# Kernel optimization log

Hardware: AMD Instinct MI355X
Metric: run time of the kernel (lower is better)

## Reference

```python
import jax, jax.numpy as jnp
import numpy as np

N_NODES = 400000
N_EDGES = 800000
N_GRAPHS = 16384
IN_DIM = 78
GNN_DIMS = [128, 128, 128]
FF_DIMS = [256, 128]


def _glorot(key, shape):
    fan_in, fan_out = shape
    lim = np.sqrt(6.0 / (fan_in + fan_out))
    return jax.random.uniform(key, shape, jnp.float32, -lim, lim)


def setup_inputs() -> dict:
    key = jax.random.key(0)
    ks = jax.random.split(key, 16)
    x = jax.random.normal(ks[0], (N_NODES, IN_DIM), jnp.float32)
    edge_index = jax.random.randint(ks[1], (2, N_EDGES), 0, N_NODES, jnp.int64)
    batch = jnp.sort(jax.random.randint(ks[2], (N_NODES,), 0, N_GRAPHS, jnp.int64))
    d = dict(x=x, edge_index=edge_index, batch=batch, n_graphs=N_GRAPHS)
    dims = [IN_DIM] + GNN_DIMS
    for i in range(3):
        d[f'gW{i}'] = _glorot(ks[3 + i], (dims[i], dims[i + 1]))
        d[f'gb{i}'] = jnp.zeros((dims[i + 1],), jnp.float32)
    fdims = [GNN_DIMS[-1]] + FF_DIMS
    for i in range(2):
        d[f'fW{i}'] = _glorot(ks[8 + i], (fdims[i], fdims[i + 1]))
        d[f'fb{i}'] = jnp.zeros((fdims[i + 1],), jnp.float32)
    return d


def gcn_conv(x, src, dst, deg_isqrt, W, b, n_nodes):
    # GCNConv: linear first, then propagate with sym norm over A + I
    h = x @ W  # [N, D]
    norm = (deg_isqrt[src] * deg_isqrt[dst])[:, None]  # [E, 1]
    msg = h[src] * norm  # [E, D] gather
    out = jax.ops.segment_sum(msg, dst, num_segments=n_nodes)  # scatter-add
    # self-loop contribution: norm_ii = deg_i^-1
    out = out + h * (deg_isqrt * deg_isqrt)[:, None]
    return out + b


def reference(x, edge_index, batch, n_graphs,
              gW0, gb0, gW1, gb1, gW2, gb2,
              fW0, fb0, fW1, fb1):
    n_nodes = x.shape[0]
    src, dst = edge_index[0], edge_index[1]
    # degree of A + I on target side
    deg = 1.0 + jax.ops.segment_sum(jnp.ones((src.shape[0],), x.dtype), dst,
                                    num_segments=n_nodes)
    deg_isqrt = jax.lax.rsqrt(deg)
    for W, b in ((gW0, gb0), (gW1, gb1), (gW2, gb2)):
        x = jax.nn.relu(gcn_conv(x, src, dst, deg_isqrt, W, b, n_nodes))
    # global max pool per graph (empty segments -> 0; x >= 0 post-ReLU)
    pooled = jax.ops.segment_max(x, batch, num_segments=n_graphs)
    pooled = jnp.where(jnp.isfinite(pooled), pooled, 0.0)
    # FF head: Linear -> ReLU -> Dropout(eval: identity)
    h = jax.nn.relu(pooled @ fW0 + fb0)
    h = jax.nn.relu(h @ fW1 + fb1)
    return h
```

## Files before the change

kernel.cpp:

```cpp
#include <hip/hip_runtime.h>

#define NN 400000
#define NE 800000
#define NG 16384

typedef short bf16x8 __attribute__((ext_vector_type(8)));
typedef float f32x4 __attribute__((ext_vector_type(4)));
typedef unsigned short u16x8 __attribute__((ext_vector_type(8)));

static inline int cdiv(int a, int b) { return (a + b - 1) / b; }

__device__ inline unsigned short bf16_rne(float v) {
    unsigned u = __float_as_uint(v);
    unsigned r = u + 0x7FFFu + ((u >> 16) & 1u);
    return (unsigned short)(r >> 16);
}
__device__ inline float bf16_to_f(unsigned short h) {
    return __uint_as_float(((unsigned)h) << 16);
}
__device__ inline void split2(float v, unsigned short& hi, unsigned short& lo) {
    hi = bf16_rne(v);
    lo = bf16_rne(v - bf16_to_f(hi));
}

__global__ __launch_bounds__(256) void fill_kernel(float* __restrict__ p, float v, int n) {
    int i = blockIdx.x * blockDim.x + threadIdx.x;
    if (i < n) p[i] = v;
}

__global__ __launch_bounds__(256) void fill_int_kernel(int* __restrict__ p, int v, int n) {
    int i = blockIdx.x * blockDim.x + threadIdx.x;
    if (i < n) p[i] = v;
}

__global__ __launch_bounds__(256) void hist_kernel(const int* __restrict__ dst,
                                                   int* __restrict__ deg, int E) {
    int e = blockIdx.x * blockDim.x + threadIdx.x;
    if (e < E) atomicAdd(&deg[dst[e]], 1);
}

__global__ __launch_bounds__(256) void disq_kernel(const int* __restrict__ deg,
                                                   float* __restrict__ disq, int n) {
    int i = blockIdx.x * blockDim.x + threadIdx.x;
    if (i < n) disq[i] = rsqrtf(1.0f + (float)deg[i]);
}

#define SCAN_TPB 256
#define SCAN_EPT 8
#define SCAN_BE (SCAN_TPB * SCAN_EPT)

__global__ __launch_bounds__(SCAN_TPB) void scan_a_kernel(const int* __restrict__ in,
                                                          int* __restrict__ out,
                                                          int* __restrict__ partials, int n) {
    __shared__ int sums[SCAN_TPB];
    const int tid = threadIdx.x;
    int base = blockIdx.x * SCAN_BE + tid * SCAN_EPT;
    int v[SCAN_EPT];
    int s = 0;
#pragma unroll
    for (int i = 0; i < SCAN_EPT; ++i) {
        int idx = base + i;
        int x = (idx < n) ? in[idx] : 0;
        v[i] = s;
        s += x;
    }
    sums[tid] = s;
    __syncthreads();
    for (int off = 1; off < SCAN_TPB; off <<= 1) {
        int t = (tid >= off) ? sums[tid - off] : 0;
        __syncthreads();
        sums[tid] += t;
        __syncthreads();
    }
    int toff = (tid == 0) ? 0 : sums[tid - 1];
#pragma unroll
    for (int i = 0; i < SCAN_EPT; ++i) {
        int idx = base + i;
        if (idx < n) out[idx] = toff + v[i];
    }
    if (tid == SCAN_TPB - 1) partials[blockIdx.x] = sums[SCAN_TPB - 1];
}

__global__ void scan_b_kernel(int* __restrict__ partials, int nb) {
    if (blockIdx.x == 0 && threadIdx.x == 0) {
        int s = 0;
        for (int i = 0; i < nb; ++i) { int x = partials[i]; partials[i] = s; s += x; }
    }
}

__global__ __launch_bounds__(256) void scan_c_kernel(int* __restrict__ out,
                                                     const int* __restrict__ partials, int n) {
    int idx = blockIdx.x * blockDim.x + threadIdx.x;
    if (idx < n) out[idx] += partials[idx / SCAN_BE];
}

__global__ __launch_bounds__(256) void csr_fill_kernel(const int* __restrict__ src,
                                                       const int* __restrict__ dst,
                                                       const int* __restrict__ rowptr,
                                                       int* __restrict__ cnt,
                                                       const float* __restrict__ disq,
                                                       int2* __restrict__ csr_ent, int E) {
    int e = blockIdx.x * blockDim.x + threadIdx.x;
    if (e >= E) return;
    int d = dst[e], s = src[e];
    int pos = rowptr[d] + atomicAdd(&cnt[d], 1);
    csr_ent[pos] = make_int2(s, __float_as_int(disq[s] * disq[d]));
}

__global__ __launch_bounds__(256) void prep_w_kernel(const float* __restrict__ W, int K,
                                                     unsigned short* __restrict__ planeHi,
                                                     unsigned short* __restrict__ planeLo) {
    int i = blockIdx.x * blockDim.x + threadIdx.x;
    if (i >= 128 * 128) return;
    int n = i >> 7, k = i & 127;
    float v = (k < K) ? W[k * 128 + n] : 0.0f;
    unsigned short hi, lo;
    split2(v, hi, lo);
    int elem = (n * 256 + ((2 * k) ^ ((n & 7) << 4))) >> 1;
    planeHi[elem] = hi;
    planeLo[elem] = lo;
}

__global__ __launch_bounds__(256) void xconv_kernel(const float* __restrict__ x,
                                                    unsigned short* __restrict__ xbf) {
    long long t = (long long)blockIdx.x * blockDim.x + threadIdx.x;
    if (t >= (long long)NN * 96) return;
    int node = (int)(t / 96), k = (int)(t - (long long)node * 96);
    float v = (k < 78) ? x[(size_t)node * 78 + k] : 0.0f;
    xbf[(size_t)node * 96 + k] = bf16_rne(v);
}

template <int STRIDE>
__global__ __launch_bounds__(256) void gather_kernel(const unsigned short* __restrict__ act,
                                                     const int* __restrict__ rowptr,
                                                     const int* __restrict__ deg,
                                                     const int2* __restrict__ csr_ent,
                                                     const float* __restrict__ disq,
                                                     unsigned short* __restrict__ aggHi, int n) {
    int t = blockIdx.x * blockDim.x + threadIdx.x;
    if (t >= n * 16) return;
    int node = t >> 4, q = (t & 15) * 8;
    const bool live = q < STRIDE;
    const int qc = live ? q : 0;
    int beg = rowptr[node];
    int d = deg[node];
    float si = disq[node];
    float s2 = si * si;
    u16x8 su = *reinterpret_cast<const u16x8*>(act + (size_t)node * STRIDE + qc);
    float acc[8];
#pragma unroll
    for (int i = 0; i < 8; ++i) acc[i] = bf16_to_f(su[i]) * s2;
    if (d > 0) {
        int lim = d - 1;
        int2 e[6];
#pragma unroll
        for (int j = 0; j < 6; ++j) e[j] = csr_ent[beg + (j < lim ? j : lim)];
        u16x8 u[6];
        float nr[6];
#pragma unroll
        for (int j = 0; j < 6; ++j) {
            u[j] = *reinterpret_cast<const u16x8*>(act + (size_t)e[j].x * STRIDE + qc);
            nr[j] = (j < d) ? __int_as_float(e[j].y) : 0.0f;
        }
#pragma unroll
        for (int j = 0; j < 6; ++j)
#pragma unroll
            for (int i = 0; i < 8; ++i) acc[i] = fmaf(bf16_to_f(u[j][i]), nr[j], acc[i]);
        for (int j = 6; j < d; ++j) {
            int2 ee = csr_ent[beg + j];
            float nn = __int_as_float(ee.y);
            u16x8 uu = *reinterpret_cast<const u16x8*>(act + (size_t)ee.x * STRIDE + qc);
#pragma unroll
            for (int i = 0; i < 8; ++i) acc[i] = fmaf(bf16_to_f(uu[i]), nn, acc[i]);
        }
    }
    if (live) {
        u16x8 h8;
#pragma unroll
        for (int i = 0; i < 8; ++i) h8[i] = bf16_rne(acc[i]);
        *reinterpret_cast<u16x8*>(aggHi + (size_t)node * STRIDE + q) = h8;
    }
}

template <int NKC, int AS>
__global__ __launch_bounds__(256) void gemm_mfma_kernel(const unsigned short* __restrict__ A,
                                                        const unsigned short* __restrict__ WT,
                                                        const float* __restrict__ bias,
                                                        unsigned short* __restrict__ act, int M) {
    __shared__ unsigned short lds[2 * 128 * 128];
    const int tid = threadIdx.x;
    {
        const unsigned* s = reinterpret_cast<const unsigned*>(WT);
        unsigned* d = reinterpret_cast<unsigned*>(lds);
#pragma unroll
        for (int i = 0; i < 64; ++i) d[tid + 256 * i] = s[tid + 256 * i];
    }
    __syncthreads();

    const int w = tid >> 6, lane = tid & 63;
    const int m = lane & 15, kb = lane >> 4;
    const char* ldsHiB = reinterpret_cast<const char*>(lds);
    const char* ldsLoB = ldsHiB + 128 * 256;

    float bcol[8];
#pragma unroll
    for (int ct = 0; ct < 8; ++ct) bcol[ct] = bias[ct * 16 + m];

    const int RT = 4;
    for (int rt = 0; rt < RT; ++rt) {
        int row0 = (blockIdx.x * RT + rt) * 64;
        if (row0 >= M) return;
        int arow = row0 + w * 16 + m;

        bf16x8 ah[NKC];
#pragma unroll
        for (int kc = 0; kc < NKC; ++kc)
            ah[kc] = *reinterpret_cast<const bf16x8*>(A + (size_t)arow * AS + kc * 32 + kb * 8);

        f32x4 acc[8];
#pragma unroll
        for (int ct = 0; ct < 8; ++ct)
#pragma unroll
            for (int r = 0; r < 4; ++r) acc[ct][r] = 0.0f;

#pragma unroll
        for (int ct = 0; ct < 8; ++ct) {
            int n = ct * 16 + m;
            int swz = (n & 7) << 4;
            int rowb = n * 256;
#pragma unroll
            for (int kc = 0; kc < NKC; ++kc) {
                int bb = rowb + ((kc * 64 + kb * 16) ^ swz);
                bf16x8 bh = *reinterpret_cast<const bf16x8*>(ldsHiB + bb);
                bf16x8 bl = *reinterpret_cast<const bf16x8*>(ldsLoB + bb);
                acc[ct] = __builtin_amdgcn_mfma_f32_16x16x32_bf16(ah[kc], bh, acc[ct], 0, 0, 0);
                acc[ct] = __builtin_amdgcn_mfma_f32_16x16x32_bf16(ah[kc], bl, acc[ct], 0, 0, 0);
            }
        }

        unsigned short* ap = act + (size_t)(row0 + w * 16) * 128;
#pragma unroll
        for (int ct = 0; ct < 8; ++ct)
#pragma unroll
            for (int r = 0; r < 4; ++r) {
                float v = fmaxf(acc[ct][r] + bcol[ct], 0.0f);
                ap[(size_t)(kb * 4 + r) * 128 + ct * 16 + m] = bf16_rne(v);
            }
    }
}

template <bool RELU_A, bool EPI>
__global__ __launch_bounds__(256) void gemm_kernel(const float* __restrict__ A,
                                                   const float* __restrict__ B,
                                                   const float* __restrict__ bias,
                                                   float* __restrict__ C,
                                                   int M, int N, int K) {
    const int BM = 64, BN = 64, BK = 16;
    __shared__ float As[BK][BM + 4];
    __shared__ float Bs[BK][BN + 4];

    const int tid = threadIdx.x;
    const int bm = blockIdx.x * BM;
    const int bn = blockIdx.y * BN;
    const int tx = tid & 15;
    const int ty = tid >> 4;

    const int arow = tid >> 2;
    const int acol = (tid & 3) * 4;
    const int brow = tid >> 4;
    const int bcol = (tid & 15) * 4;

    float acc[4][4] = {};

    for (int k0 = 0; k0 < K; k0 += BK) {
        {
            const float* ap = A + (size_t)(bm + arow) * K;
#pragma unroll
            for (int j = 0; j < 4; ++j) {
                int kk = k0 + acol + j;
                float v = (kk < K) ? ap[kk] : 0.0f;
                if (RELU_A) v = fmaxf(v, 0.0f);
                As[acol + j][arow] = v;
            }
        }
        {
            int kk = k0 + brow;
            float4 v = make_float4(0.f, 0.f, 0.f, 0.f);
            if (kk < K) v = *reinterpret_cast<const float4*>(B + (size_t)kk * N + bn + bcol);
            *reinterpret_cast<float4*>(&Bs[brow][bcol]) = v;
        }
        __syncthreads();
#pragma unroll
        for (int k = 0; k < BK; ++k) {
            float4 a4 = *reinterpret_cast<const float4*>(&As[k][ty * 4]);
            float4 b4 = *reinterpret_cast<const float4*>(&Bs[k][tx * 4]);
            float av[4] = {a4.x, a4.y, a4.z, a4.w};
            float bv[4] = {b4.x, b4.y, b4.z, b4.w};
#pragma unroll
            for (int i = 0; i < 4; ++i)
#pragma unroll
                for (int j = 0; j < 4; ++j)
                    acc[i][j] = fmaf(av[i], bv[j], acc[i][j]);
        }
        __syncthreads();
    }

    const int crow0 = bm + ty * 4;
    const int ccol0 = bn + tx * 4;
    float4 bv = make_float4(0.f, 0.f, 0.f, 0.f);
    if (EPI) bv = *reinterpret_cast<const float4*>(bias + ccol0);
#pragma unroll
    for (int i = 0; i < 4; ++i) {
        float4 v = make_float4(acc[i][0], acc[i][1], acc[i][2], acc[i][3]);
        if (EPI) {
            v.x = fmaxf(v.x + bv.x, 0.f);
            v.y = fmaxf(v.y + bv.y, 0.f);
            v.z = fmaxf(v.z + bv.z, 0.f);
            v.w = fmaxf(v.w + bv.w, 0.f);
        }
        *reinterpret_cast<float4*>(C + (size_t)(crow0 + i) * N + ccol0) = v;
    }
}

__global__ __launch_bounds__(256) void pool_kernel(const unsigned short* __restrict__ act,
                                                   const int* __restrict__ batch,
                                                   int* __restrict__ pooled, int n) {
    int t = blockIdx.x * blockDim.x + threadIdx.x;
    int d = t & 127;
    int n0 = (t >> 7) * 8;
    if (n0 >= n) return;
    int cur = batch[n0];
    float m = fmaxf(bf16_to_f(act[(size_t)n0 * 128 + d]), 0.f);
    for (int i = 1; i < 8 && (n0 + i) < n; ++i) {
        int b = batch[n0 + i];
        float v = fmaxf(bf16_to_f(act[(size_t)(n0 + i) * 128 + d]), 0.f);
        if (b == cur) {
            m = fmaxf(m, v);
        } else {
            atomicMax(&pooled[cur * 128 + d], __float_as_int(m));
            cur = b;
            m = v;
        }
    }
    atomicMax(&pooled[cur * 128 + d], __float_as_int(m));
}

extern "C" void kernel_launch(void* const* d_in, const int* in_sizes, int n_in,
                              void* d_out, int out_size, void* d_ws, size_t ws_size,
                              hipStream_t stream) {
    const float* x    = (const float*)d_in[0];
    const int*   edge = (const int*)d_in[1];
    const int*   batch= (const int*)d_in[2];
    const float* gW0  = (const float*)d_in[4];
    const float* gb0  = (const float*)d_in[5];
    const float* gW1  = (const float*)d_in[6];
    const float* gb1  = (const float*)d_in[7];
    const float* gW2  = (const float*)d_in[8];
    const float* gb2  = (const float*)d_in[9];
    const float* fW0  = (const float*)d_in[10];
    const float* fb0  = (const float*)d_in[11];
    const float* fW1  = (const float*)d_in[12];
    const float* fb1  = (const float*)d_in[13];
    float* out = (float*)d_out;

    unsigned short* actB  = (unsigned short*)d_ws;
    unsigned short* aggHi = actB + (size_t)NN * 128;
    float* disq   = (float*)(aggHi + (size_t)NN * 128);
    float* pooled = disq + NN;
    float* ffh    = pooled + (size_t)NG * 128;
    int*   deg    = (int*)(ffh + (size_t)NG * 256);
    int*   rowptr = deg + NN;
    int2*  csr_ent = (int2*)(rowptr + NN);
    unsigned short* wt0 = (unsigned short*)(csr_ent + NE);
    unsigned short* wt1 = wt0 + 2 * 128 * 128;
    unsigned short* wt2 = wt1 + 2 * 128 * 128;
    int* partials = (int*)(wt2 + 2 * 128 * 128);
    int* cnt = (int*)pooled;
    unsigned short* xbf = actB;

    const int* src = edge;
    const int* dst = edge + NE;

    fill_int_kernel<<<cdiv(NN, 256), 256, 0, stream>>>(deg, 0, NN);
    fill_int_kernel<<<cdiv(NN, 256), 256, 0, stream>>>(cnt, 0, NN);
    hist_kernel<<<cdiv(NE, 256), 256, 0, stream>>>(dst, deg, NE);
    disq_kernel<<<cdiv(NN, 256), 256, 0, stream>>>(deg, disq, NN);
    int nsb = cdiv(NN, SCAN_BE);
    scan_a_kernel<<<nsb, SCAN_TPB, 0, stream>>>(deg, rowptr, partials, NN);
    scan_b_kernel<<<1, 64, 0, stream>>>(partials, nsb);
    scan_c_kernel<<<cdiv(NN, 256), 256, 0, stream>>>(rowptr, partials, NN);
    csr_fill_kernel<<<cdiv(NE, 256), 256, 0, stream>>>(src, dst, rowptr, cnt, disq,
                                                       csr_ent, NE);
    prep_w_kernel<<<64, 256, 0, stream>>>(gW0, 78, wt0, wt0 + 128 * 128);
    prep_w_kernel<<<64, 256, 0, stream>>>(gW1, 128, wt1, wt1 + 128 * 128);
    prep_w_kernel<<<64, 256, 0, stream>>>(gW2, 128, wt2, wt2 + 128 * 128);
    xconv_kernel<<<cdiv(NN * 96, 256), 256, 0, stream>>>(x, xbf);

    const int gemm_blocks = cdiv(NN / 64, 4);
    const int gather_blocks = cdiv(NN * 16, 256);

    gather_kernel<96><<<gather_blocks, 256, 0, stream>>>(xbf, rowptr, deg, csr_ent, disq,
                                                         aggHi, NN);
    gemm_mfma_kernel<3, 96><<<gemm_blocks, 256, 0, stream>>>(aggHi, wt0, gb0, actB, NN);
    gather_kernel<128><<<gather_blocks, 256, 0, stream>>>(actB, rowptr, deg, csr_ent, disq,
                                                          aggHi, NN);
    gemm_mfma_kernel<4, 128><<<gemm_blocks, 256, 0, stream>>>(aggHi, wt1, gb1, actB, NN);
    gather_kernel<128><<<gather_blocks, 256, 0, stream>>>(actB, rowptr, deg, csr_ent, disq,
                                                          aggHi, NN);
    gemm_mfma_kernel<4, 128><<<gemm_blocks, 256, 0, stream>>>(aggHi, wt2, gb2, actB, NN);

    fill_kernel<<<cdiv(NG * 128, 256), 256, 0, stream>>>(pooled, 0.0f, NG * 128);
    pool_kernel<<<cdiv(cdiv(NN, 8) * 128, 256), 256, 0, stream>>>(actB, batch, (int*)pooled, NN);

    gemm_kernel<false, true><<<dim3(NG / 64, 4), 256, 0, stream>>>(pooled, fW0, fb0, ffh, NG, 256, 128);
    gemm_kernel<false, true><<<dim3(NG / 64, 2), 256, 0, stream>>>(ffh, fW1, fb1, out, NG, 128, 256);
}
```

Before: 627.5 us.

## Run FF head GEMMs on bf16 MFMA split-weight kernel and vectorize input conversion

Replaces the fp32 SIMT tiled GEMM for the two feed-forward layers with the existing bf16 hi/lo split-weight MFMA kernel. The 256-wide dimensions are split into two 128x128 weight tiles, and new epilogue modes write fp32 partials and then add them for the second layer. The pooled values and the hidden activations are rounded to bf16, which adds precision loss. The x-to-bf16 conversion now handles four elements per thread with vector stores.

```diff
diff --git a/kernel.cpp b/kernel.cpp
--- a/kernel.cpp
+++ b/kernel.cpp
@@ -107,13 +107,15 @@
     csr_ent[pos] = make_int2(s, __float_as_int(disq[s] * disq[d]));
 }
 
-__global__ __launch_bounds__(256) void prep_w_kernel(const float* __restrict__ W, int K,
+__global__ __launch_bounds__(256) void prep_w_kernel(const float* __restrict__ W,
+                                                     int Ktot, int Ntot, int k0, int n0,
                                                      unsigned short* __restrict__ planeHi,
                                                      unsigned short* __restrict__ planeLo) {
     int i = blockIdx.x * blockDim.x + threadIdx.x;
     if (i >= 128 * 128) return;
     int n = i >> 7, k = i & 127;
-    float v = (k < K) ? W[k * 128 + n] : 0.0f;
+    int gk = k0 + k, gn = n0 + n;
+    float v = (gk < Ktot && gn < Ntot) ? W[(size_t)gk * Ntot + gn] : 0.0f;
     unsigned short hi, lo;
     split2(v, hi, lo);
     int elem = (n * 256 + ((2 * k) ^ ((n & 7) << 4))) >> 1;
@@ -123,11 +125,27 @@
 
 __global__ __launch_bounds__(256) void xconv_kernel(const float* __restrict__ x,
                                                     unsigned short* __restrict__ xbf) {
-    long long t = (long long)blockIdx.x * blockDim.x + threadIdx.x;
-    if (t >= (long long)NN * 96) return;
-    int node = (int)(t / 96), k = (int)(t - (long long)node * 96);
-    float v = (k < 78) ? x[(size_t)node * 78 + k] : 0.0f;
-    xbf[(size_t)node * 96 + k] = bf16_rne(v);
+    int t = blockIdx.x * blockDim.x + threadIdx.x;
+    if (t >= NN * 24) return;
+    int node = t / 24;
+    int q = (t - node * 24) * 4;
+    const float* xp = x + (size_t)node * 78;
+    ushort4 o;
+    o.x = bf16_rne((q + 0 < 78) ? xp[q + 0] : 0.0f);
+    o.y = bf16_rne((q + 1 < 78) ? xp[q + 1] : 0.0f);
+    o.z = bf16_rne((q + 2 < 78) ? xp[q + 2] : 0.0f);
+    o.w = bf16_rne((q + 3 < 78) ? xp[q + 3] : 0.0f);
+    *reinterpret_cast<ushort4*>(xbf + (size_t)node * 96 + q) = o;
+}
+
+__global__ __launch_bounds__(256) void f2bf_kernel(const float* __restrict__ in,
+                                                   unsigned short* __restrict__ o, int n4) {
+    int i = blockIdx.x * blockDim.x + threadIdx.x;
+    if (i >= n4) return;
+    float4 v = *reinterpret_cast<const float4*>(in + i * 4);
+    ushort4 u;
+    u.x = bf16_rne(v.x); u.y = bf16_rne(v.y); u.z = bf16_rne(v.z); u.w = bf16_rne(v.w);
+    *reinterpret_cast<ushort4*>(o + i * 4) = u;
 }
 
 template <int STRIDE>
@@ -182,11 +200,14 @@
     }
 }
 
-template <int NKC, int AS>
+template <int NKC, int AS, int MODE>
 __global__ __launch_bounds__(256) void gemm_mfma_kernel(const unsigned short* __restrict__ A,
                                                         const unsigned short* __restrict__ WT,
                                                         const float* __restrict__ bias,
-                                                        unsigned short* __restrict__ act, int M) {
+                                                        unsigned short* __restrict__ actout,
+                                                        float* __restrict__ f32out,
+                                                        const float* __restrict__ partial,
+                                                        int M, int a_k0, int ostride, int ocol) {
     __shared__ unsigned short lds[2 * 128 * 128];
     const int tid = threadIdx.x;
     {
@@ -203,8 +224,10 @@
     const char* ldsLoB = ldsHiB + 128 * 256;
 
     float bcol[8];
-#pragma unroll
-    for (int ct = 0; ct < 8; ++ct) bcol[ct] = bias[ct * 16 + m];
+    if (MODE != 1) {
+#pragma unroll
+        for (int ct = 0; ct < 8; ++ct) bcol[ct] = bias[ct * 16 + m];
+    }
 
     const int RT = 4;
     for (int rt = 0; rt < RT; ++rt) {
@@ -215,7 +238,7 @@
         bf16x8 ah[NKC];
 #pragma unroll
         for (int kc = 0; kc < NKC; ++kc)
-            ah[kc] = *reinterpret_cast<const bf16x8*>(A + (size_t)arow * AS + kc * 32 + kb * 8);
+            ah[kc] = *reinterpret_cast<const bf16x8*>(A + (size_t)arow * AS + a_k0 + kc * 32 + kb * 8);
 
         f32x4 acc[8];
 #pragma unroll
@@ -238,87 +261,34 @@
             }
         }
 
-        unsigned short* ap = act + (size_t)(row0 + w * 16) * 128;
-#pragma unroll
-        for (int ct = 0; ct < 8; ++ct)
-#pragma unroll
-            for (int r = 0; r < 4; ++r) {
-                float v = fmaxf(acc[ct][r] + bcol[ct], 0.0f);
-                ap[(size_t)(kb * 4 + r) * 128 + ct * 16 + m] = bf16_rne(v);
-            }
-    }
-}
-
-template <bool RELU_A, bool EPI>
-__global__ __launch_bounds__(256) void gemm_kernel(const float* __restrict__ A,
-                                                   const float* __restrict__ B,
-                                                   const float* __restrict__ bias,
-                                                   float* __restrict__ C,
-                                                   int M, int N, int K) {
-    const int BM = 64, BN = 64, BK = 16;
-    __shared__ float As[BK][BM + 4];
-    __shared__ float Bs[BK][BN + 4];
-
-    const int tid = threadIdx.x;
-    const int bm = blockIdx.x * BM;
-    const int bn = blockIdx.y * BN;
-    const int tx = tid & 15;
-    const int ty = tid >> 4;
-
-    const int arow = tid >> 2;
-    const int acol = (tid & 3) * 4;
-    const int brow = tid >> 4;
-    const int bcol = (tid & 15) * 4;
-
-    float acc[4][4] = {};
-
-    for (int k0 = 0; k0 < K; k0 += BK) {
-        {
-            const float* ap = A + (size_t)(bm + arow) * K;
-#pragma unroll
-            for (int j = 0; j < 4; ++j) {
-                int kk = k0 + acol + j;
-                float v = (kk < K) ? ap[kk] : 0.0f;
-                if (RELU_A) v = fmaxf(v, 0.0f);
-                As[acol + j][arow] = v;
-            }
+        if (MODE == 0) {
+            unsigned short* ap = actout + (size_t)(row0 + w * 16) * ostride + ocol;
+#pragma unroll
+            for (int ct = 0; ct < 8; ++ct)
+#pragma unroll
+                for (int r = 0; r < 4; ++r) {
+                    float v = fmaxf(acc[ct][r] + bcol[ct], 0.0f);
+                    ap[(size_t)(kb * 4 + r) * ostride + ct * 16 + m] = bf16_rne(v);
+                }
+        } else if (MODE == 1) {
+            float* fp = f32out + (size_t)(row0 + w * 16) * 128;
+#pragma unroll
+            for (int ct = 0; ct < 8; ++ct)
+#pragma unroll
+                for (int r = 0; r < 4; ++r)
+                    fp[(size_t)(kb * 4 + r) * 128 + ct * 16 + m] = acc[ct][r];
+        } else {
+            const float* pp = partial + (size_t)(row0 + w * 16) * 128;
+            float* fp = f32out + (size_t)(row0 + w * 16) * 128;
+#pragma unroll
+            for (int ct = 0; ct < 8; ++ct)
+#pragma unroll
+                for (int r = 0; r < 4; ++r) {
+                    size_t idx = (size_t)(kb * 4 + r) * 128 + ct * 16 + m;
+                    float v = fmaxf(acc[ct][r] + pp[idx] + bcol[ct], 0.0f);
+                    fp[idx] = v;
+                }
         }
-        {
-            int kk = k0 + brow;
-            float4 v = make_float4(0.f, 0.f, 0.f, 0.f);
-            if (kk < K) v = *reinterpret_cast<const float4*>(B + (size_t)kk * N + bn + bcol);
-            *reinterpret_cast<float4*>(&Bs[brow][bcol]) = v;
-        }
-        __syncthreads();
-#pragma unroll
-        for (int k = 0; k < BK; ++k) {
-            float4 a4 = *reinterpret_cast<const float4*>(&As[k][ty * 4]);
-            float4 b4 = *reinterpret_cast<const float4*>(&Bs[k][tx * 4]);
-            float av[4] = {a4.x, a4.y, a4.z, a4.w};
-            float bv[4] = {b4.x, b4.y, b4.z, b4.w};
-#pragma unroll
-            for (int i = 0; i < 4; ++i)
-#pragma unroll
-                for (int j = 0; j < 4; ++j)
-                    acc[i][j] = fmaf(av[i], bv[j], acc[i][j]);
-        }
-        __syncthreads();
-    }
-
-    const int crow0 = bm + ty * 4;
-    const int ccol0 = bn + tx * 4;
-    float4 bv = make_float4(0.f, 0.f, 0.f, 0.f);
-    if (EPI) bv = *reinterpret_cast<const float4*>(bias + ccol0);
-#pragma unroll
-    for (int i = 0; i < 4; ++i) {
-        float4 v = make_float4(acc[i][0], acc[i][1], acc[i][2], acc[i][3]);
-        if (EPI) {
-            v.x = fmaxf(v.x + bv.x, 0.f);
-            v.y = fmaxf(v.y + bv.y, 0.f);
-            v.z = fmaxf(v.z + bv.z, 0.f);
-            v.w = fmaxf(v.w + bv.w, 0.f);
-        }
-        *reinterpret_cast<float4*>(C + (size_t)(crow0 + i) * N + ccol0) = v;
     }
 }
 
@@ -367,14 +337,19 @@
     unsigned short* aggHi = actB + (size_t)NN * 128;
     float* disq   = (float*)(aggHi + (size_t)NN * 128);
     float* pooled = disq + NN;
-    float* ffh    = pooled + (size_t)NG * 128;
-    int*   deg    = (int*)(ffh + (size_t)NG * 256);
+    unsigned short* pooledbf = (unsigned short*)(pooled + (size_t)NG * 128);
+    unsigned short* ffhbf    = pooledbf + (size_t)NG * 128;
+    int*   deg    = (int*)(ffhbf + (size_t)NG * 256);
     int*   rowptr = deg + NN;
     int2*  csr_ent = (int2*)(rowptr + NN);
-    unsigned short* wt0 = (unsigned short*)(csr_ent + NE);
-    unsigned short* wt1 = wt0 + 2 * 128 * 128;
-    unsigned short* wt2 = wt1 + 2 * 128 * 128;
-    int* partials = (int*)(wt2 + 2 * 128 * 128);
+    unsigned short* wt0  = (unsigned short*)(csr_ent + NE);
+    unsigned short* wt1  = wt0 + 2 * 128 * 128;
+    unsigned short* wt2  = wt1 + 2 * 128 * 128;
+    unsigned short* wtF0a = wt2 + 2 * 128 * 128;
+    unsigned short* wtF0b = wtF0a + 2 * 128 * 128;
+    unsigned short* wtF1a = wtF0b + 2 * 128 * 128;
+    unsigned short* wtF1b = wtF1a + 2 * 128 * 128;
+    int* partials = (int*)(wtF1b + 2 * 128 * 128);
     int* cnt = (int*)pooled;
     unsigned short* xbf = actB;
 
@@ -391,27 +366,42 @@
     scan_c_kernel<<<cdiv(NN, 256), 256, 0, stream>>>(rowptr, partials, NN);
     csr_fill_kernel<<<cdiv(NE, 256), 256, 0, stream>>>(src, dst, rowptr, cnt, disq,
                                                        csr_ent, NE);
-    prep_w_kernel<<<64, 256, 0, stream>>>(gW0, 78, wt0, wt0 + 128 * 128);
-    prep_w_kernel<<<64, 256, 0, stream>>>(gW1, 128, wt1, wt1 + 128 * 128);
-    prep_w_kernel<<<64, 256, 0, stream>>>(gW2, 128, wt2, wt2 + 128 * 128);
-    xconv_kernel<<<cdiv(NN * 96, 256), 256, 0, stream>>>(x, xbf);
+    prep_w_kernel<<<64, 256, 0, stream>>>(gW0, 78, 128, 0, 0, wt0, wt0 + 128 * 128);
+    prep_w_kernel<<<64, 256, 0, stream>>>(gW1, 128, 128, 0, 0, wt1, wt1 + 128 * 128);
+    prep_w_kernel<<<64, 256, 0, stream>>>(gW2, 128, 128, 0, 0, wt2, wt2 + 128 * 128);
+    prep_w_kernel<<<64, 256, 0, stream>>>(fW0, 128, 256, 0, 0,   wtF0a, wtF0a + 128 * 128);
+    prep_w_kernel<<<64, 256, 0, stream>>>(fW0, 128, 256, 0, 128, wtF0b, wtF0b + 128 * 128);
+    prep_w_kernel<<<64, 256, 0, stream>>>(fW1, 256, 128, 0, 0,   wtF1a, wtF1a + 128 * 128);
+    prep_w_kernel<<<64, 256, 0, stream>>>(fW1, 256, 128, 128, 0, wtF1b, wtF1b + 128 * 128);
+    xconv_kernel<<<cdiv(NN * 24, 256), 256, 0, stream>>>(x, xbf);
 
     const int gemm_blocks = cdiv(NN / 64, 4);
     const int gather_blocks = cdiv(NN * 16, 256);
+    const int ff_blocks = NG / 256;
 
     gather_kernel<96><<<gather_blocks, 256, 0, stream>>>(xbf, rowptr, deg, csr_ent, disq,
                                                          aggHi, NN);
-    gemm_mfma_kernel<3, 96><<<gemm_blocks, 256, 0, stream>>>(aggHi, wt0, gb0, actB, NN);
+    gemm_mfma_kernel<3, 96, 0><<<gemm_blocks, 256, 0, stream>>>(
+        aggHi, wt0, gb0, actB, nullptr, nullptr, NN, 0, 128, 0);
     gather_kernel<128><<<gather_blocks, 256, 0, stream>>>(actB, rowptr, deg, csr_ent, disq,
                                                           aggHi, NN);
-    gemm_mfma_kernel<4, 128><<<gemm_blocks, 256, 0, stream>>>(aggHi, wt1, gb1, actB, NN);
+    gemm_mfma_kernel<4, 128, 0><<<gemm_blocks, 256, 0, stream>>>(
+        aggHi, wt1, gb1, actB, nullptr, nullptr, NN, 0, 128, 0);
     gather_kernel<128><<<gather_blocks, 256, 0, stream>>>(actB, rowptr, deg, csr_ent, disq,
                                                           aggHi, NN);
-    gemm_mfma_kernel<4, 128><<<gemm_blocks, 256, 0, stream>>>(aggHi, wt2, gb2, actB, NN);
+    gemm_mfma_kernel<4, 128, 0><<<gemm_blocks, 256, 0, stream>>>(
+        aggHi, wt2, gb2, actB, nullptr, nullptr, NN, 0, 128, 0);
 
     fill_kernel<<<cdiv(NG * 128, 256), 256, 0, stream>>>(pooled, 0.0f, NG * 128);
     pool_kernel<<<cdiv(cdiv(NN, 8) * 128, 256), 256, 0, stream>>>(actB, batch, (int*)pooled, NN);
-
-    gemm_kernel<false, true><<<dim3(NG / 64, 4), 256, 0, stream>>>(pooled, fW0, fb0, ffh, NG, 256, 128);
-    gemm_kernel<false, true><<<dim3(NG / 64, 2), 256, 0, stream>>>(ffh, fW1, fb1, out, NG, 128, 256);
-}
+    f2bf_kernel<<<cdiv(NG * 32, 256), 256, 0, stream>>>(pooled, pooledbf, NG * 32);
+
+    gemm_mfma_kernel<4, 128, 0><<<ff_blocks, 256, 0, stream>>>(
+        pooledbf, wtF0a, fb0, ffhbf, nullptr, nullptr, NG, 0, 256, 0);
+    gemm_mfma_kernel<4, 128, 0><<<ff_blocks, 256, 0, stream>>>(
+        pooledbf, wtF0b, fb0 + 128, ffhbf, nullptr, nullptr, NG, 0, 256, 128);
+    gemm_mfma_kernel<4, 256, 1><<<ff_blocks, 256, 0, stream>>>(
+        ffhbf, wtF1a, nullptr, nullptr, pooled, nullptr, NG, 0, 128, 0);
+    gemm_mfma_kernel<4, 256, 2><<<ff_blocks, 256, 0, stream>>>(
+        ffhbf, wtF1b, fb1, nullptr, out, pooled, NG, 128, 128, 0);
+}
```

After: 597.8 us, median of 2. -4.7%, faster.
